# Kernel optimization log

Measured on AMD Instinct MI355X. Metric: run time of the kernel, lower is better.

Reference implementation:

```python
import jax, jax.numpy as jnp
import numpy as np

KERNEL = 8


def setup_inputs() -> dict:
    key = jax.random.key(0)
    ks = jax.random.split(key, 9)
    N, Cin, L = 16, 128, 2048
    Cout = 256
    x = jax.random.normal(ks[0], (N, Cin, L), dtype=jnp.float32)
    conv_w = jax.random.normal(ks[1], (Cout, Cin, KERNEL), dtype=jnp.float32) * (1.0 / np.sqrt(Cin * KERNEL))
    conv_b = jax.random.normal(ks[2], (Cout,), dtype=jnp.float32) * 0.01
    wq = jax.random.normal(ks[3], (Cout, Cout), dtype=jnp.float32) * (1.0 / np.sqrt(Cout))
    bq = jax.random.normal(ks[4], (Cout,), dtype=jnp.float32) * 0.01
    wk = jax.random.normal(ks[5], (Cout, Cout), dtype=jnp.float32) * (1.0 / np.sqrt(Cout))
    bk = jax.random.normal(ks[6], (Cout,), dtype=jnp.float32) * 0.01
    wv = jax.random.normal(ks[7], (Cout, Cout), dtype=jnp.float32) * (1.0 / np.sqrt(Cout))
    bv = jax.random.normal(ks[8], (Cout,), dtype=jnp.float32) * 0.01
    return {"x": x, "conv_w": conv_w, "conv_b": conv_b,
            "wq": wq, "bq": bq, "wk": wk, "bk": bk, "wv": wv, "bv": bv}


def reference(x, conv_w, conv_b, wq, bq, wk, bk, wv, bv):
    # Conv1d, valid padding: [N, Cin, L] -> [N, Cout, S], S = L - KERNEL + 1
    h = jax.lax.conv_general_dilated(
        x, conv_w, window_strides=(1,), padding='VALID',
        dimension_numbers=('NCH', 'OIH', 'NCH'))
    h = jax.nn.relu(h + conv_b[None, :, None])
    N, C, S = h.shape
    h = jnp.transpose(h, (0, 2, 1))  # [N, S, C]
    # Linear layers (torch convention: y = x @ W^T + b)
    q = jnp.einsum('nsc,dc->nsd', h, wq) + bq
    k = jnp.einsum('nsc,dc->nsd', h, wk) + bk
    v = jnp.einsum('nsc,dc->nsd', h, wv) + bv
    # sigmoid (non-normalized) attention over full SxS scores
    scores = jnp.einsum('nsd,ntd->nst', q, k) / jnp.sqrt(jnp.asarray(C, h.dtype))
    attn = jax.nn.sigmoid(scores)  # [N, S, S]
    out = jnp.einsum('nst,ntd->nsd', attn, v)
    return jnp.transpose(out, (0, 2, 1))  # [N, C, S]
```

## Files before the change

### kernel.cpp

```cpp
#include <hip/hip_runtime.h>

typedef short short8 __attribute__((ext_vector_type(8)));
typedef float f32x4 __attribute__((ext_vector_type(4)));
typedef float f32x16 __attribute__((ext_vector_type(16)));
typedef unsigned short u16x4 __attribute__((ext_vector_type(4)));

constexpr int NB = 16, CIN = 128, LIN = 2048, CO = 256;
constexpr int SL = 2041;
constexpr int MT = NB * SL;
constexpr int MP = 32768;
constexpr int XTS = 136;

constexpr size_t XT_OFF = 0;
constexpr size_t XT_SZ  = (size_t)NB*LIN*XTS*2 + 65536;
constexpr size_t CW_OFF = XT_OFF + XT_SZ;
constexpr size_t CW_SZ  = (size_t)CO*CIN*8*2;
constexpr size_t WQ_OFF = CW_OFF + CW_SZ;
constexpr size_t WB_SZ  = (size_t)CO*CO*2;
constexpr size_t WK_OFF = WQ_OFF + WB_SZ;
constexpr size_t WV_OFF = WK_OFF + WB_SZ;
constexpr size_t H_OFF  = WV_OFF + WB_SZ;
constexpr size_t HB_SZ  = (size_t)MP*CO*2;
constexpr size_t Q_OFF  = H_OFF + HB_SZ;
constexpr size_t K_OFF  = Q_OFF + HB_SZ;
constexpr size_t VT_OFF = K_OFF + HB_SZ;

__device__ inline unsigned short f2bf(float f) {
  union { float f; unsigned int u; } v; v.f = f;
  unsigned int r = v.u + 0x7fffu + ((v.u >> 16) & 1u);
  return (unsigned short)(r >> 16);
}

__device__ inline void sync_lds() {
  __asm__ volatile("" ::: "memory");
  __builtin_amdgcn_s_waitcnt(0xc07f);
  __builtin_amdgcn_s_barrier();
  __asm__ volatile("" ::: "memory");
}
__device__ inline void barrier_only() {
  __asm__ volatile("" ::: "memory");
  __builtin_amdgcn_s_barrier();
  __asm__ volatile("" ::: "memory");
}

#if defined(__has_builtin)
#if __has_builtin(__builtin_amdgcn_global_load_lds)
#define HAVE_GLDS 1
#endif
#endif

__device__ inline void gld16(const unsigned short* g, void* l) {
#ifdef HAVE_GLDS
  __builtin_amdgcn_global_load_lds(
      (const __attribute__((address_space(1))) void*)g,
      (__attribute__((address_space(3))) void*)l, 16, 0, 0);
#else
  *(short8*)l = *(const short8*)g;
#endif
}

__device__ inline unsigned int cvt_pk_bf16(float a, float b) {
  unsigned int r;
  asm("v_cvt_pk_bf16_f32 %0, %1, %2" : "=v"(r) : "v"(a), "v"(b));
  return r;
}
__device__ inline void swap32(unsigned int& a, unsigned int& b) {
  asm("v_permlane32_swap_b32 %0, %1" : "+v"(a), "+v"(b));
}

__global__ void xpose_kernel(const float* __restrict__ x, unsigned short* __restrict__ xt) {
  __shared__ float tile[32][33];
  const int tx = threadIdx.x, ty = threadIdx.y;
  const int s0 = blockIdx.x * 32, c0 = blockIdx.y * 32, n = blockIdx.z;
  #pragma unroll
  for (int r = 0; r < 4; ++r)
    tile[ty * 4 + r][tx] = x[((size_t)(n * CIN + c0 + ty * 4 + r)) * LIN + s0 + tx];
  __syncthreads();
  #pragma unroll
  for (int r = 0; r < 4; ++r)
    xt[((size_t)(n * LIN + s0 + ty * 4 + r)) * XTS + c0 + tx] = f2bf(tile[tx][ty * 4 + r]);
}

__global__ void wconv_kernel(const float* __restrict__ w, unsigned short* __restrict__ o) {
  int idx = blockIdx.x * 256 + threadIdx.x;
  int co = idx >> 10, r = idx & 1023, kp = r >> 7, ci = r & 127;
  o[idx] = f2bf(w[co * 1024 + ci * 8 + kp]);
}

__global__ void wqkv_kernel(const float* __restrict__ a, const float* __restrict__ b,
                            const float* __restrict__ c, unsigned short* __restrict__ oa,
                            unsigned short* __restrict__ ob, unsigned short* __restrict__ oc) {
  int z = blockIdx.x >> 6, lb = blockIdx.x & 63;
  const float* src = (z == 0) ? a : (z == 1) ? b : c;
  unsigned short* dst = (z == 0) ? oa : (z == 1) ? ob : oc;
  int i = (lb * 256 + threadIdx.x) * 4;
  float4 v = *(const float4*)(src + i);
  u16x4 r;
  r.x = f2bf(v.x); r.y = f2bf(v.y); r.z = f2bf(v.z); r.w = f2bf(v.w);
  *(u16x4*)(dst + i) = r;
}

__global__ __launch_bounds__(256) void conv_gemm(
    const unsigned short* __restrict__ xt,
    const unsigned short* __restrict__ wb,
    const float* __restrict__ bias,
    unsigned short* __restrict__ h)
{
  __shared__ unsigned short sX[18432];
  __shared__ unsigned short sB[2][4096];
  const int tid = threadIdx.x;
  const int w = tid >> 6, lane = tid & 63, quad = lane >> 4, l16 = lane & 15;
  const int n  = blockIdx.y;
  const int s0 = blockIdx.x * 128;
  const int d0 = blockIdx.z * 128;

  {
    const unsigned short* xbase = xt + ((size_t)n * LIN + s0) * XTS;
    #pragma unroll
    for (int i = 0; i < 9; ++i) {
      int u = i * 256 + tid;
      gld16(xbase + u * 8, ((char*)sX) + u * 16);
    }
  }

  const int brow0 = tid >> 2, bkgs = tid & 3;
  short8 breg[2];
  #pragma unroll
  for (int i2 = 0; i2 < 2; ++i2) {
    int row = i2 * 64 + brow0;
    int kg = bkgs ^ ((row >> 1) & 3);
    breg[i2] = *(const short8*)(wb + (size_t)(d0 + row) * 1024 + kg * 8);
  }
  #pragma unroll
  for (int i2 = 0; i2 < 2; ++i2)
    *(short8*)(&sB[0][(i2 * 256 + tid) * 8]) = breg[i2];
  __syncthreads();

  f32x4 acc[2][8];
  #pragma unroll
  for (int i = 0; i < 2; ++i)
    #pragma unroll
    for (int j = 0; j < 8; ++j) acc[i][j] = (f32x4){0.f, 0.f, 0.f, 0.f};

  for (int kc = 0; kc < 32; ++kc) {
    const int kcn = (kc < 31) ? kc + 1 : kc;
    const int kpn = kcn >> 2, ci0n = (kcn & 3) * 32;
    #pragma unroll
    for (int i2 = 0; i2 < 2; ++i2) {
      int row = i2 * 64 + brow0;
      int kg = bkgs ^ ((row >> 1) & 3);
      breg[i2] = *(const short8*)(wb + (size_t)(d0 + row) * 1024 + kpn * 128 + ci0n + kg * 8);
    }

    const int kp = kc >> 2, ci0 = (kc & 3) * 32;
    const unsigned short* sBc = sB[kc & 1];
    short8 bfr[8];
    #pragma unroll
    for (int j = 0; j < 8; ++j) {
      int r = j * 16 + l16;
      bfr[j] = *(const short8*)(sBc + r * 32 + (quad ^ ((r >> 1) & 3)) * 8);
    }
    #pragma unroll
    for (int i = 0; i < 2; ++i) {
      int srow = w * 32 + i * 16 + l16;
      short8 afr = *(const short8*)(sX + (srow + kp) * XTS + ci0 + quad * 8);
      #pragma unroll
      for (int j = 0; j < 8; ++j)
        acc[i][j] = __builtin_amdgcn_mfma_f32_16x16x32_bf16(afr, bfr[j], acc[i][j], 0, 0, 0);
    }

    #pragma unroll
    for (int i2 = 0; i2 < 2; ++i2)
      *(short8*)(&sB[(kc + 1) & 1][(i2 * 256 + tid) * 8]) = breg[i2];
    sync_lds();
  }

  #pragma unroll
  for (int i = 0; i < 2; ++i)
    #pragma unroll
    for (int j = 0; j < 8; ++j) {
      int col = d0 + j * 16 + l16;
      float bv = bias[col];
      #pragma unroll
      for (int jj = 0; jj < 4; ++jj) {
        int s = s0 + w * 32 + i * 16 + quad * 4 + jj;
        if (s < SL) {
          float val = fmaxf(acc[i][j][jj] + bv, 0.f);
          h[(size_t)(n * SL + s) * CO + col] = f2bf(val);
        }
      }
    }
}

__global__ __launch_bounds__(256) void lin_gemm(
    const unsigned short* __restrict__ A,
    const unsigned short* __restrict__ Bq, const unsigned short* __restrict__ Bk,
    const unsigned short* __restrict__ Bv,
    const float* __restrict__ biq, const float* __restrict__ bik,
    const float* __restrict__ biv,
    unsigned short* __restrict__ qb, unsigned short* __restrict__ kb,
    unsigned short* __restrict__ vtb)
{
  __shared__ unsigned short sA[2][4096];
  __shared__ unsigned short sB[2][4096];
  const int tid = threadIdx.x;
  const int w = tid >> 6, lane = tid & 63, quad = lane >> 4, l16 = lane & 15;
  const int m0 = blockIdx.x * 128, d0 = blockIdx.y * 128, z = blockIdx.z;
  const unsigned short* B = (z == 0) ? Bq : (z == 1) ? Bk : Bv;
  const float* bias        = (z == 0) ? biq : (z == 1) ? bik : biv;

  const int brow0 = tid >> 2, bkgs = tid & 3;
  short8 areg[2], breg[2];
  #pragma unroll
  for (int i2 = 0; i2 < 2; ++i2) {
    int row = i2 * 64 + brow0;
    int kg = bkgs ^ ((row >> 1) & 3);
    areg[i2] = *(const short8*)(A + (size_t)(m0 + row) * CO + kg * 8);
    breg[i2] = *(const short8*)(B + (size_t)(d0 + row) * CO + kg * 8);
  }
  #pragma unroll
  for (int i2 = 0; i2 < 2; ++i2) {
    *(short8*)(&sA[0][(i2 * 256 + tid) * 8]) = areg[i2];
    *(short8*)(&sB[0][(i2 * 256 + tid) * 8]) = breg[i2];
  }
  sync_lds();

  f32x4 acc[2][8];
  #pragma unroll
  for (int i = 0; i < 2; ++i)
    #pragma unroll
    for (int j = 0; j < 8; ++j) acc[i][j] = (f32x4){0.f, 0.f, 0.f, 0.f};

  for (int kc = 0; kc < 8; ++kc) {
    const int kcn = (kc < 7) ? kc + 1 : kc;
    #pragma unroll
    for (int i2 = 0; i2 < 2; ++i2) {
      int row = i2 * 64 + brow0;
      int kg = bkgs ^ ((row >> 1) & 3);
      areg[i2] = *(const short8*)(A + (size_t)(m0 + row) * CO + kcn * 32 + kg * 8);
      breg[i2] = *(const short8*)(B + (size_t)(d0 + row) * CO + kcn * 32 + kg * 8);
    }

    const unsigned short* sAc = sA[kc & 1];
    const unsigned short* sBc = sB[kc & 1];
    short8 afr[2], bfr[8];
    #pragma unroll
    for (int i = 0; i < 2; ++i) {
      int r = w * 32 + i * 16 + l16;
      afr[i] = *(const short8*)(sAc + r * 32 + (quad ^ ((r >> 1) & 3)) * 8);
    }
    #pragma unroll
    for (int j = 0; j < 8; ++j) {
      int r = j * 16 + l16;
      bfr[j] = *(const short8*)(sBc + r * 32 + (quad ^ ((r >> 1) & 3)) * 8);
    }
    #pragma unroll
    for (int i = 0; i < 2; ++i)
      #pragma unroll
      for (int j = 0; j < 8; ++j)
        acc[i][j] = __builtin_amdgcn_mfma_f32_16x16x32_bf16(afr[i], bfr[j], acc[i][j], 0, 0, 0);

    #pragma unroll
    for (int i2 = 0; i2 < 2; ++i2) {
      *(short8*)(&sA[(kc + 1) & 1][(i2 * 256 + tid) * 8]) = areg[i2];
      *(short8*)(&sB[(kc + 1) & 1][(i2 * 256 + tid) * 8]) = breg[i2];
    }
    sync_lds();
  }

  #pragma unroll
  for (int i = 0; i < 2; ++i)
    #pragma unroll
    for (int j = 0; j < 8; ++j) {
      int col = d0 + j * 16 + l16;
      float bv = bias[col];
      #pragma unroll
      for (int jj = 0; jj < 4; ++jj) {
        int m = m0 + w * 32 + i * 16 + quad * 4 + jj;
        float val = acc[i][j][jj] + bv;
        if (z == 0) {
          qb[(size_t)m * CO + col] = f2bf(val * 0.0625f);
        } else if (z == 1) {
          kb[(size_t)m * CO + col] = f2bf(val);
        } else if (m < MT) {
          int nn = m / SL, ss = m - nn * SL;
          vtb[(size_t)col * MP + nn * 2048 + ss] = f2bf(val);
        }
      }
    }
}

__global__ __launch_bounds__(256, 1) void attn_kernel(
    const unsigned short* __restrict__ qb,
    const unsigned short* __restrict__ kb,
    const unsigned short* __restrict__ vtb,
    float* __restrict__ out)
{
  __shared__ unsigned short sK[2][16384];
  __shared__ unsigned short sV[2][16384];
  const int tid = threadIdx.x;
  const int w = tid >> 6, lane = tid & 63;
  const int half = lane >> 5, l32 = lane & 31;
  const int bidx = blockIdx.x;
  const int n = (bidx & 7) + ((bidx >> 7) << 3);
  const int s0 = ((bidx >> 3) & 15) * 128;

  const unsigned short* kbN = kb + (size_t)(n * SL) * CO;
  const unsigned short* vbN = vtb + (size_t)n * 2048;

#define STAGE_TILE(buf, tk)                                                      \
  {                                                                              \
    _Pragma("unroll")                                                            \
    for (int i = 0; i < 8; ++i) {                                                \
      int u = i * 256 + tid;                                                     \
      int t = u >> 5, sl = u & 31;                                               \
      gld16(kbN + (size_t)((tk) + t) * CO + ((sl ^ (t & 31)) << 3),              \
            ((char*)sK[buf]) + u * 16);                                          \
    }                                                                            \
    _Pragma("unroll")                                                            \
    for (int i = 0; i < 8; ++i) {                                                \
      int u = i * 256 + tid;                                                     \
      int d = u >> 3, sl = u & 7;                                                \
      gld16(vbN + (size_t)d * MP + (tk) + ((sl ^ (d & 7)) << 3),                 \
            ((char*)sV[buf]) + u * 16);                                          \
    }                                                                            \
  }

  STAGE_TILE(0, 0)

  short8 qf[16];
  {
    const unsigned short* qp = qb + (size_t)(n * SL + s0 + w * 32 + l32) * CO + half * 8;
    #pragma unroll
    for (int kk = 0; kk < 16; ++kk) qf[kk] = *(const short8*)(qp + kk * 16);
  }

  __builtin_amdgcn_s_waitcnt(0x0F70);
  barrier_only();

  f32x16 o[8];
  #pragma unroll
  for (int di = 0; di < 8; ++di)
    #pragma unroll
    for (int r = 0; r < 16; ++r) o[di][r] = 0.f;

  for (int it = 0; it < 32; ++it) {
    const int cur = it & 1;
    if (it < 31) STAGE_TILE(cur ^ 1, (it + 1) * 64)

    const unsigned short* sKc = sK[cur];
    const unsigned short* sVc = sV[cur];

    #pragma unroll
    for (int th = 0; th < 2; ++th) {
      const int tl = th * 32 + l32;
      f32x16 sacc;
      #pragma unroll
      for (int r = 0; r < 16; ++r) sacc[r] = 0.f;
      __builtin_amdgcn_s_setprio(1);
      #pragma unroll
      for (int kk = 0; kk < 16; ++kk) {
        short8 kf = *(const short8*)(sKc + tl * 256 + (((kk * 2 + half) ^ (tl & 31)) << 3));
        sacc = __builtin_amdgcn_mfma_f32_32x32x16_bf16(kf, qf[kk], sacc, 0, 0, 0);
      }
      __builtin_amdgcn_s_setprio(0);

      #pragma unroll
      for (int r = 0; r < 16; ++r)
        sacc[r] = __builtin_amdgcn_rcpf(1.f + __expf(-sacc[r]));
      if (it == 31 && th == 1) {
        #pragma unroll
        for (int r = 0; r < 16; ++r) {
          int tloc = (r & 3) + 8 * (r >> 2) + 4 * half;
          if (tloc >= 25) sacc[r] = 0.f;
        }
      }

      short8 pa[2];
      #pragma unroll
      for (int kx = 0; kx < 2; ++kx) {
        unsigned int x0 = cvt_pk_bf16(sacc[kx * 8 + 0], sacc[kx * 8 + 1]);
        unsigned int x1 = cvt_pk_bf16(sacc[kx * 8 + 2], sacc[kx * 8 + 3]);
        unsigned int y0 = cvt_pk_bf16(sacc[kx * 8 + 4], sacc[kx * 8 + 5]);
        unsigned int y1 = cvt_pk_bf16(sacc[kx * 8 + 6], sacc[kx * 8 + 7]);
        swap32(x0, y0);
        swap32(x1, y1);
        union { unsigned int u[4]; short8 s; } pu;
        pu.u[0] = x0; pu.u[1] = x1; pu.u[2] = y0; pu.u[3] = y1;
        pa[kx] = pu.s;
      }

      __builtin_amdgcn_s_setprio(1);
      #pragma unroll
      for (int kx = 0; kx < 2; ++kx) {
        const int c8 = th * 4 + kx * 2 + half;
        #pragma unroll
        for (int di = 0; di < 8; ++di) {
          int d = di * 32 + l32;
          short8 vf = *(const short8*)(sVc + d * 64 + ((c8 ^ (d & 7)) << 3));
          o[di] = __builtin_amdgcn_mfma_f32_32x32x16_bf16(vf, pa[kx], o[di], 0, 0, 0);
        }
      }
      __builtin_amdgcn_s_setprio(0);
    }

    if (it < 31) __builtin_amdgcn_s_waitcnt(0x0F70);
    sync_lds();
  }

  const int s = s0 + w * 32 + l32;
  if (s < SL) {
    float* op = out + (size_t)n * CO * SL + s;
    #pragma unroll
    for (int di = 0; di < 8; ++di)
      #pragma unroll
      for (int r = 0; r < 16; ++r) {
        int d = di * 32 + (r & 3) + 8 * (r >> 2) + 4 * half;
        __builtin_nontemporal_store(o[di][r], op + (size_t)d * SL);
      }
  }
#undef STAGE_TILE
}

extern "C" void kernel_launch(void* const* d_in, const int* in_sizes, int n_in,
                              void* d_out, int out_size, void* d_ws, size_t ws_size,
                              hipStream_t stream) {
  const float* x      = (const float*)d_in[0];
  const float* conv_w = (const float*)d_in[1];
  const float* conv_b = (const float*)d_in[2];
  const float* wq     = (const float*)d_in[3];
  const float* bq     = (const float*)d_in[4];
  const float* wk     = (const float*)d_in[5];
  const float* bk     = (const float*)d_in[6];
  const float* wv     = (const float*)d_in[7];
  const float* bv     = (const float*)d_in[8];

  char* ws = (char*)d_ws;
  unsigned short* xt  = (unsigned short*)(ws + XT_OFF);
  unsigned short* cw  = (unsigned short*)(ws + CW_OFF);
  unsigned short* wqb = (unsigned short*)(ws + WQ_OFF);
  unsigned short* wkb = (unsigned short*)(ws + WK_OFF);
  unsigned short* wvb = (unsigned short*)(ws + WV_OFF);
  unsigned short* hb  = (unsigned short*)(ws + H_OFF);
  unsigned short* qb  = (unsigned short*)(ws + Q_OFF);
  unsigned short* kb  = (unsigned short*)(ws + K_OFF);
  unsigned short* vtb = (unsigned short*)(ws + VT_OFF);

  hipLaunchKernelGGL(xpose_kernel, dim3(64, 4, 16), dim3(32, 8), 0, stream, x, xt);
  hipLaunchKernelGGL(wconv_kernel, dim3(1024), dim3(256), 0, stream, conv_w, cw);
  hipLaunchKernelGGL(wqkv_kernel,  dim3(192), dim3(256), 0, stream,
                     wq, wk, wv, wqb, wkb, wvb);
  hipLaunchKernelGGL(conv_gemm, dim3(16, 16, 2), dim3(256), 0, stream, xt, cw, conv_b, hb);
  hipLaunchKernelGGL(lin_gemm,  dim3(256, 2, 3), dim3(256), 0, stream,
                     hb, wqb, wkb, wvb, bq, bk, bv, qb, kb, vtb);
  hipLaunchKernelGGL(attn_kernel, dim3(256), dim3(256), 0, stream,
                     qb, kb, vtb, (float*)d_out);
}
```

Measured before the change: 259.3 us.

## Shrink attention blocks to two waves and drop LDS double buffering

Splits the attention work into 512 blocks of 128 threads, each covering 64 query rows and 32-key tiles, with a single-buffered LDS stage for K and V. Launch bounds now allow two blocks per CU, so more waves are resident to hide latency and the grid fills the 256 CUs twice. In exchange, loading the next tile is serialized behind compute with two barriers per iteration, there are twice as many loop trips, and each block must reload K and V for fewer query rows.

Result: slower. 438.6 us (+69.2%).

```diff
diff --git a/kernel.cpp b/kernel.cpp
--- a/kernel.cpp
+++ b/kernel.cpp
@@ -290,43 +290,43 @@
     }
 }
 
-__global__ __launch_bounds__(256, 1) void attn_kernel(
+__global__ __launch_bounds__(128, 2) void attn_kernel(
     const unsigned short* __restrict__ qb,
     const unsigned short* __restrict__ kb,
     const unsigned short* __restrict__ vtb,
     float* __restrict__ out)
 {
-  __shared__ unsigned short sK[2][16384];
-  __shared__ unsigned short sV[2][16384];
+  __shared__ unsigned short sK[8192];
+  __shared__ unsigned short sV[8192];
   const int tid = threadIdx.x;
   const int w = tid >> 6, lane = tid & 63;
   const int half = lane >> 5, l32 = lane & 31;
   const int bidx = blockIdx.x;
-  const int n = (bidx & 7) + ((bidx >> 7) << 3);
-  const int s0 = ((bidx >> 3) & 15) * 128;
+  const int n = (bidx & 7) + ((bidx >> 8) << 3);
+  const int s0 = ((bidx >> 3) & 31) * 64;
 
   const unsigned short* kbN = kb + (size_t)(n * SL) * CO;
   const unsigned short* vbN = vtb + (size_t)n * 2048;
 
-#define STAGE_TILE(buf, tk)                                                      \
+#define STAGE_TILE(tk)                                                           \
   {                                                                              \
     _Pragma("unroll")                                                            \
     for (int i = 0; i < 8; ++i) {                                                \
-      int u = i * 256 + tid;                                                     \
+      int u = i * 128 + tid;                                                     \
       int t = u >> 5, sl = u & 31;                                               \
       gld16(kbN + (size_t)((tk) + t) * CO + ((sl ^ (t & 31)) << 3),              \
-            ((char*)sK[buf]) + u * 16);                                          \
+            ((char*)sK) + u * 16);                                               \
     }                                                                            \
     _Pragma("unroll")                                                            \
     for (int i = 0; i < 8; ++i) {                                                \
-      int u = i * 256 + tid;                                                     \
-      int d = u >> 3, sl = u & 7;                                                \
-      gld16(vbN + (size_t)d * MP + (tk) + ((sl ^ (d & 7)) << 3),                 \
-            ((char*)sV[buf]) + u * 16);                                          \
+      int u = i * 128 + tid;                                                     \
+      int d = u >> 2, sl = u & 3;                                                \
+      gld16(vbN + (size_t)d * MP + (tk) + ((sl ^ (d & 3)) << 3),                 \
+            ((char*)sV) + u * 16);                                               \
     }                                                                            \
   }
 
-  STAGE_TILE(0, 0)
+  STAGE_TILE(0)
 
   short8 qf[16];
   {
@@ -344,68 +344,62 @@
     #pragma unroll
     for (int r = 0; r < 16; ++r) o[di][r] = 0.f;
 
-  for (int it = 0; it < 32; ++it) {
-    const int cur = it & 1;
-    if (it < 31) STAGE_TILE(cur ^ 1, (it + 1) * 64)
-
-    const unsigned short* sKc = sK[cur];
-    const unsigned short* sVc = sV[cur];
-
-    #pragma unroll
-    for (int th = 0; th < 2; ++th) {
-      const int tl = th * 32 + l32;
-      f32x16 sacc;
-      #pragma unroll
-      for (int r = 0; r < 16; ++r) sacc[r] = 0.f;
-      __builtin_amdgcn_s_setprio(1);
-      #pragma unroll
-      for (int kk = 0; kk < 16; ++kk) {
-        short8 kf = *(const short8*)(sKc + tl * 256 + (((kk * 2 + half) ^ (tl & 31)) << 3));
-        sacc = __builtin_amdgcn_mfma_f32_32x32x16_bf16(kf, qf[kk], sacc, 0, 0, 0);
+  for (int it = 0; it < 64; ++it) {
+    f32x16 sacc;
+    #pragma unroll
+    for (int r = 0; r < 16; ++r) sacc[r] = 0.f;
+    __builtin_amdgcn_s_setprio(1);
+    #pragma unroll
+    for (int kk = 0; kk < 16; ++kk) {
+      short8 kf = *(const short8*)(sK + l32 * 256 + (((kk * 2 + half) ^ l32) << 3));
+      sacc = __builtin_amdgcn_mfma_f32_32x32x16_bf16(kf, qf[kk], sacc, 0, 0, 0);
+    }
+    __builtin_amdgcn_s_setprio(0);
+
+    #pragma unroll
+    for (int r = 0; r < 16; ++r)
+      sacc[r] = __builtin_amdgcn_rcpf(1.f + __expf(-sacc[r]));
+    if (it == 63) {
+      #pragma unroll
+      for (int r = 0; r < 16; ++r) {
+        int tloc = (r & 3) + 8 * (r >> 2) + 4 * half;
+        if (tloc >= 25) sacc[r] = 0.f;
       }
-      __builtin_amdgcn_s_setprio(0);
-
-      #pragma unroll
-      for (int r = 0; r < 16; ++r)
-        sacc[r] = __builtin_amdgcn_rcpf(1.f + __expf(-sacc[r]));
-      if (it == 31 && th == 1) {
-        #pragma unroll
-        for (int r = 0; r < 16; ++r) {
-          int tloc = (r & 3) + 8 * (r >> 2) + 4 * half;
-          if (tloc >= 25) sacc[r] = 0.f;
-        }
+    }
+
+    short8 pa[2];
+    #pragma unroll
+    for (int kx = 0; kx < 2; ++kx) {
+      unsigned int x0 = cvt_pk_bf16(sacc[kx * 8 + 0], sacc[kx * 8 + 1]);
+      unsigned int x1 = cvt_pk_bf16(sacc[kx * 8 + 2], sacc[kx * 8 + 3]);
+      unsigned int y0 = cvt_pk_bf16(sacc[kx * 8 + 4], sacc[kx * 8 + 5]);
+      unsigned int y1 = cvt_pk_bf16(sacc[kx * 8 + 6], sacc[kx * 8 + 7]);
+      swap32(x0, y0);
+      swap32(x1, y1);
+      union { unsigned int u[4]; short8 s; } pu;
+      pu.u[0] = x0; pu.u[1] = x1; pu.u[2] = y0; pu.u[3] = y1;
+      pa[kx] = pu.s;
+    }
+
+    __builtin_amdgcn_s_setprio(1);
+    #pragma unroll
+    for (int kx = 0; kx < 2; ++kx) {
+      const int c4 = kx * 2 + half;
+      #pragma unroll
+      for (int di = 0; di < 8; ++di) {
+        int d = di * 32 + l32;
+        short8 vf = *(const short8*)(sV + d * 32 + ((c4 ^ (d & 3)) << 3));
+        o[di] = __builtin_amdgcn_mfma_f32_32x32x16_bf16(vf, pa[kx], o[di], 0, 0, 0);
       }
-
-      short8 pa[2];
-      #pragma unroll
-      for (int kx = 0; kx < 2; ++kx) {
-        unsigned int x0 = cvt_pk_bf16(sacc[kx * 8 + 0], sacc[kx * 8 + 1]);
-        unsigned int x1 = cvt_pk_bf16(sacc[kx * 8 + 2], sacc[kx * 8 + 3]);
-        unsigned int y0 = cvt_pk_bf16(sacc[kx * 8 + 4], sacc[kx * 8 + 5]);
-        unsigned int y1 = cvt_pk_bf16(sacc[kx * 8 + 6], sacc[kx * 8 + 7]);
-        swap32(x0, y0);
-        swap32(x1, y1);
-        union { unsigned int u[4]; short8 s; } pu;
-        pu.u[0] = x0; pu.u[1] = x1; pu.u[2] = y0; pu.u[3] = y1;
-        pa[kx] = pu.s;
-      }
-
-      __builtin_amdgcn_s_setprio(1);
-      #pragma unroll
-      for (int kx = 0; kx < 2; ++kx) {
-        const int c8 = th * 4 + kx * 2 + half;
-        #pragma unroll
-        for (int di = 0; di < 8; ++di) {
-          int d = di * 32 + l32;
-          short8 vf = *(const short8*)(sVc + d * 64 + ((c8 ^ (d & 7)) << 3));
-          o[di] = __builtin_amdgcn_mfma_f32_32x32x16_bf16(vf, pa[kx], o[di], 0, 0, 0);
-        }
-      }
-      __builtin_amdgcn_s_setprio(0);
-    }
-
-    if (it < 31) __builtin_amdgcn_s_waitcnt(0x0F70);
+    }
+    __builtin_amdgcn_s_setprio(0);
+
     sync_lds();
+    if (it < 63) {
+      STAGE_TILE((it + 1) * 32)
+      __builtin_amdgcn_s_waitcnt(0x0F70);
+    }
+    barrier_only();
   }
 
   const int s = s0 + w * 32 + l32;
@@ -453,6 +447,6 @@
   hipLaunchKernelGGL(conv_gemm, dim3(16, 16, 2), dim3(256), 0, stream, xt, cw, conv_b, hb);
   hipLaunchKernelGGL(lin_gemm,  dim3(256, 2, 3), dim3(256), 0, stream,
                      hb, wqb, wkb, wvb, bq, bk, bv, qb, kb, vtb);
-  hipLaunchKernelGGL(attn_kernel, dim3(256), dim3(256), 0, stream,
+  hipLaunchKernelGGL(attn_kernel, dim3(512), dim3(128), 0, stream,
                      qb, kb, vtb, (float*)d_out);
 }
```
